# Kernel optimization log

Hardware: AMD Instinct MI355X
Metric: run time of the kernel (lower is better)

## Reference

```python
import jax, jax.numpy as jnp
import numpy as np

K = 3          # kernel size
KF = K * K     # kernel field = 9
PAD = 1
STRIDE = 1


def _conv(x, w, b):
    y = jax.lax.conv_general_dilated(
        x, w, (STRIDE, STRIDE), [(PAD, PAD), (PAD, PAD)],
        dimension_numbers=('NCHW', 'OIHW', 'NCHW'))
    return y + b[None, :, None, None]


def _bilinear_gather(x, py, px):
    # x: [B,C,H,W]; py/px: [B,KF,Ho,Wo] float sampling coords (zero-pad outside)
    B, C, H, W = x.shape
    xf = x.reshape(B, C, H * W)
    y0 = jnp.floor(py)
    x0 = jnp.floor(px)

    def corner(yc, xc):
        wy = 1.0 - jnp.abs(py - yc)
        wx = 1.0 - jnp.abs(px - xc)
        valid = (yc >= 0) & (yc <= H - 1) & (xc >= 0) & (xc <= W - 1)
        yi = jnp.clip(yc, 0, H - 1).astype(jnp.int32)
        xi = jnp.clip(xc, 0, W - 1).astype(jnp.int32)
        idx = (yi * W + xi).reshape(B, -1)               # [B, KF*Ho*Wo]
        v = jax.vmap(lambda f, i: f[:, i])(xf, idx)      # [B, C, KF*Ho*Wo]
        wgt = (wy * wx * valid.astype(x.dtype)).reshape(B, 1, -1)
        return v * wgt

    return (corner(y0, x0) + corner(y0, x0 + 1) +
            corner(y0 + 1, x0) + corner(y0 + 1, x0 + 1))  # [B,C,KF*Ho*Wo]


def _deform_conv(x, offset, mask, w, b):
    # modulated deformable conv v2 (mmcv offset layout: [y,x] interleaved per kernel pt)
    B, C, H, W = x.shape
    Ho, Wo = mask.shape[2], mask.shape[3]
    kh, kw = jnp.meshgrid(jnp.arange(K), jnp.arange(K), indexing='ij')
    kh = kh.reshape(-1).astype(x.dtype)   # [KF]
    kw = kw.reshape(-1).astype(x.dtype)
    base_y = (jnp.arange(Ho) * STRIDE - PAD).astype(x.dtype)
    base_x = (jnp.arange(Wo) * STRIDE - PAD).astype(x.dtype)
    off = offset.reshape(B, KF, 2, Ho, Wo)
    py = base_y[None, None, :, None] + kh[None, :, None, None] + off[:, :, 0]
    px = base_x[None, None, None, :] + kw[None, :, None, None] + off[:, :, 1]
    val = _bilinear_gather(x, py, px).reshape(B, C, KF, Ho, Wo)
    val = val * mask[:, None]                             # modulate
    out = jnp.einsum('bckhw,ock->bohw', val, w.reshape(w.shape[0], C, KF))
    return out + b[None, :, None, None]


def setup_inputs() -> dict:
    key = jax.random.key(0)
    k1, k2, k3 = jax.random.split(key, 3)
    B, C, H, W = 8, 64, 128, 128
    x = jax.random.normal(k1, (B, C, H, W), dtype=jnp.float32)
    w_om = jax.random.normal(k2, (3 * KF, C, K, K), dtype=jnp.float32) * 0.02
    b_om = jnp.zeros((3 * KF,), dtype=jnp.float32)
    w_dc = jax.random.normal(k3, (64, C, K, K), dtype=jnp.float32) * 0.05
    b_dc = jnp.zeros((64,), dtype=jnp.float32)
    return {"x": x, "w_om": w_om, "b_om": b_om, "w_dc": w_dc, "b_dc": b_dc}


def reference(x, w_om, b_om, w_dc, b_dc):
    om = _conv(x, w_om, b_om)                 # [B, 3*KF, H, W]
    offset = om[:, :2 * KF]
    mask = 2.0 * jax.nn.sigmoid(om[:, 2 * KF:])
    return _deform_conv(x, offset, mask, w_dc, b_dc)
```

## Files before the change

### kernel.cpp

```cpp
#include <hip/hip_runtime.h>
#include <cmath>

#define IH 128
#define IW 128
#define NB 8

typedef __attribute__((ext_vector_type(8))) short bf16x8;
typedef __attribute__((ext_vector_type(4))) float f32x4;

union U4B8 { uint4 u; bf16x8 h; };

#define OFFM_OFF 0
#define XT_OFF   3538944
#define WTDC_OFF (3538944 + 4194304)
#define WTOM_OFF (3538944 + 4194304 + 18432)

__device__ __forceinline__ unsigned short f32_to_bf16(float f) {
    unsigned int u = __float_as_uint(f);
    u += 0x7fffu + ((u >> 16) & 1u);
    return (unsigned short)(u >> 16);
}

__global__ void transpose_weights(const float* __restrict__ w_dc,
                                  const float* __restrict__ w_om,
                                  unsigned short* __restrict__ wt_dc16,
                                  unsigned short* __restrict__ wt_om16) {
    int idx = blockIdx.x * blockDim.x + threadIdx.x;
    if (idx < 9 * 64 * 64) {
        int k = idx >> 12;
        int o = (idx >> 6) & 63;
        int c = idx & 63;
        wt_dc16[idx] = f32_to_bf16(w_dc[(o * 64 + c) * 9 + k]);
    }
    if (idx < 9 * 32 * 64) {
        int k = idx >> 11;
        int o = (idx >> 6) & 31;
        int c = idx & 63;
        wt_om16[idx] = (o < 27) ? f32_to_bf16(w_om[(o * 64 + c) * 9 + k])
                                : (unsigned short)0;
    }
}

__global__ __launch_bounds__(256) void transpose_x(
        const float* __restrict__ x, unsigned short* __restrict__ xT) {
    __shared__ float t[64 * 65];
    const int tid = threadIdx.x;
    const int blk = blockIdx.x;
    const int b = blk >> 8;
    const int rem = blk & 255;
    const int h = rem >> 1;
    const int w0 = (rem & 1) << 6;

    for (int i = tid; i < 4096; i += 256) {
        const int c = i >> 6;
        const int w = i & 63;
        t[w * 65 + c] = x[(((size_t)(b * 64 + c)) << 14) + (h << 7) + w0 + w];
    }
    __syncthreads();
    const int c2 = (tid & 31) * 2;
    ushort2* dst = (ushort2*)(xT + (((size_t)b << 20)) + ((size_t)((h << 7) + w0)) * 64 + c2);
#pragma unroll
    for (int p = 0; p < 8; ++p) {
        const int w = (tid >> 5) + p * 8;
        ushort2 u;
        u.x = f32_to_bf16(t[w * 65 + c2]);
        u.y = f32_to_bf16(t[w * 65 + c2 + 1]);
        dst[(size_t)w * 32] = u;
    }
}

__global__ __launch_bounds__(256, 4) void conv_om_mfma(
        const unsigned short* __restrict__ xT,
        const float* __restrict__ b_om,
        const unsigned short* __restrict__ wt_om16,
        float* __restrict__ offm) {
    __shared__ __align__(16) unsigned short wall[9 * 8 * 32 * 8];

    const int tid = threadIdx.x;
    for (int s = tid; s < 2304; s += 256) {
        const int k = s >> 8;
        const int r = s & 255;
        const int p = r >> 5;
        const int o = r & 31;
        ((uint4*)wall)[s] = ((const uint4*)wt_om16)[(k << 8) + (o << 3) + p];
    }
    __syncthreads();

    const int t = (blockIdx.x << 2) + (tid >> 6);
    const int b = t >> 10;
    const int rem = t & 1023;
    const int h = rem >> 3;
    const int w0 = (rem & 7) << 4;
    const int lane = tid & 63;
    const int ln15 = lane & 15;
    const int quad = lane >> 4;

    const unsigned short* xb = xT + ((size_t)b << 20);

    f32x4 acc[2] = {{0.f, 0.f, 0.f, 0.f}, {0.f, 0.f, 0.f, 0.f}};

#pragma unroll
    for (int k = 0; k < 9; ++k) {
        const int kh = k / 3;
        const int kw = k - kh * 3;
        const int y = h + kh - 1;
        const int xx = w0 + ln15 + kw - 1;
        U4B8 a0, a1;
        a0.u = make_uint4(0u, 0u, 0u, 0u);
        a1.u = make_uint4(0u, 0u, 0u, 0u);
        if (y >= 0 && y < IH && xx >= 0 && xx < IW) {
            const unsigned short* p = xb + (((size_t)((y << 7) + xx)) << 6) + (quad << 3);
            a0.u = *(const uint4*)p;
            a1.u = *(const uint4*)(p + 32);
        }
        const unsigned short* wb  = wall + (((k << 3) + quad) << 8);
        const unsigned short* wb4 = wall + (((k << 3) + quad + 4) << 8);
#pragma unroll
        for (int ot = 0; ot < 2; ++ot) {
            U4B8 b0, b1;
            b0.u = *(const uint4*)&wb [((ot << 4) + ln15) << 3];
            b1.u = *(const uint4*)&wb4[((ot << 4) + ln15) << 3];
            acc[ot] = __builtin_amdgcn_mfma_f32_16x16x32_bf16(a0.h, b0.h, acc[ot], 0, 0, 0);
            acc[ot] = __builtin_amdgcn_mfma_f32_16x16x32_bf16(a1.h, b1.h, acc[ot], 0, 0, 0);
        }
    }

#pragma unroll
    for (int ot = 0; ot < 2; ++ot) {
        const int o = (ot << 4) + ln15;
        if (o >= 27) continue;
        const float bias = b_om[o];
        float4 r;
        r.x = acc[ot][0] + bias;
        r.y = acc[ot][1] + bias;
        r.z = acc[ot][2] + bias;
        r.w = acc[ot][3] + bias;
        if (o >= 18) {
            r.x = 2.0f / (1.0f + __expf(-r.x));
            r.y = 2.0f / (1.0f + __expf(-r.y));
            r.z = 2.0f / (1.0f + __expf(-r.z));
            r.w = 2.0f / (1.0f + __expf(-r.w));
        }
        *(float4*)&offm[(((size_t)(b * 27 + o)) << 14) + (h << 7) + w0 + (quad << 2)] = r;
    }
}

__device__ __forceinline__ void corner2(const unsigned short* __restrict__ p,
                                        float wgt, float* v) {
    const uint4 a = *(const uint4*)p;
    const uint4 c = *(const uint4*)(p + 32);
    unsigned int u[8] = {a.x, a.y, a.z, a.w, c.x, c.y, c.z, c.w};
#pragma unroll
    for (int i = 0; i < 8; ++i) {
        v[2 * i]     += wgt * __uint_as_float(u[i] << 16);
        v[2 * i + 1] += wgt * __uint_as_float(u[i] & 0xffff0000u);
    }
}

__global__ __launch_bounds__(256, 2) void deform_mfma(
        const unsigned short* __restrict__ xT,
        const float* __restrict__ b_dc,
        const float* __restrict__ offm,
        const unsigned short* __restrict__ wt_dc16,
        float* __restrict__ out) {
    __shared__ __align__(16) unsigned short wall[9 * 8 * 64 * 8];

    const int tid = threadIdx.x;
    for (int s = tid; s < 4608; s += 256) {
        const int k = s >> 9;
        const int r = s & 511;
        const int p = r >> 6;
        const int o = r & 63;
        ((uint4*)wall)[s] = ((const uint4*)wt_dc16)[(k << 9) + (o << 3) + p];
    }
    __syncthreads();

    const int t = (blockIdx.x << 2) + (tid >> 6);
    const int b = t >> 10;
    const int rem = t & 1023;
    const int h = rem >> 3;
    const int w0 = (rem & 7) << 4;
    const int lane = tid & 63;
    const int ln15 = lane & 15;
    const int quad = lane >> 4;

    const unsigned short* xb = xT + ((size_t)b << 20);
    const float* ofb = offm + (((size_t)(b * 27)) << 14) + (h << 7) + w0 + ln15;

    f32x4 acc[4];
#pragma unroll
    for (int i = 0; i < 4; ++i) acc[i] = (f32x4){0.f, 0.f, 0.f, 0.f};

#pragma unroll
    for (int k = 0; k < 9; ++k) {
        const float offy = ofb[((size_t)(2 * k)) << 14];
        const float offx = ofb[((size_t)(2 * k + 1)) << 14];
        const float msk  = ofb[((size_t)(18 + k)) << 14];
        const int kh = k / 3;
        const int kw = k - kh * 3;
        const float py  = (float)(h + kh - 1) + offy;
        const float pxf = (float)(w0 + ln15 + kw - 1) + offx;
        const float y0f = floorf(py);
        const float x0f = floorf(pxf);
        const float fy = py - y0f;
        const float fx = pxf - x0f;
        const float wy0 = 1.0f - fy, wx0 = 1.0f - fx;
        const float vy0 = (y0f >= 0.0f && y0f <= 127.0f) ? 1.0f : 0.0f;
        const float vy1 = (y0f >= -1.0f && y0f <= 126.0f) ? 1.0f : 0.0f;
        const float vx0 = (x0f >= 0.0f && x0f <= 127.0f) ? 1.0f : 0.0f;
        const float vx1 = (x0f >= -1.0f && x0f <= 126.0f) ? 1.0f : 0.0f;
        const float w00 = wy0 * wx0 * vy0 * vx0;
        const float w01 = wy0 * fx  * vy0 * vx1;
        const float w10 = fy  * wx0 * vy1 * vx0;
        const float w11 = fy  * fx  * vy1 * vx1;
        const int y0i = min(max((int)y0f, 0), 127);
        const int y1i = min(max((int)y0f + 1, 0), 127);
        const int x0i = min(max((int)x0f, 0), 127);
        const int x1i = min(max((int)x0f + 1, 0), 127);

        float v[16];
#pragma unroll
        for (int i = 0; i < 16; ++i) v[i] = 0.0f;
        const int cofs = quad << 3;
        corner2(xb + ((((size_t)((y0i << 7) + x0i)) << 6) + cofs), w00, v);
        corner2(xb + ((((size_t)((y0i << 7) + x1i)) << 6) + cofs), w01, v);
        corner2(xb + ((((size_t)((y1i << 7) + x0i)) << 6) + cofs), w10, v);
        corner2(xb + ((((size_t)((y1i << 7) + x1i)) << 6) + cofs), w11, v);

        U4B8 a0, a1;
        unsigned int pk[8];
#pragma unroll
        for (int i = 0; i < 8; ++i) {
            const unsigned int lo = f32_to_bf16(v[2 * i] * msk);
            const unsigned int hi = f32_to_bf16(v[2 * i + 1] * msk);
            pk[i] = lo | (hi << 16);
        }
        a0.u = make_uint4(pk[0], pk[1], pk[2], pk[3]);
        a1.u = make_uint4(pk[4], pk[5], pk[6], pk[7]);

        const unsigned short* wb  = wall + (((k << 3) + quad) << 9);
        const unsigned short* wb4 = wall + (((k << 3) + quad + 4) << 9);
#pragma unroll
        for (int ot = 0; ot < 4; ++ot) {
            U4B8 b0, b1;
            b0.u = *(const uint4*)&wb [((ot << 4) + ln15) << 3];
            b1.u = *(const uint4*)&wb4[((ot << 4) + ln15) << 3];
            acc[ot] = __builtin_amdgcn_mfma_f32_16x16x32_bf16(a0.h, b0.h, acc[ot], 0, 0, 0);
            acc[ot] = __builtin_amdgcn_mfma_f32_16x16x32_bf16(a1.h, b1.h, acc[ot], 0, 0, 0);
        }
    }

#pragma unroll
    for (int ot = 0; ot < 4; ++ot) {
        const int o = (ot << 4) + ln15;
        const float bias = b_dc[o];
        float4 r;
        r.x = acc[ot][0] + bias;
        r.y = acc[ot][1] + bias;
        r.z = acc[ot][2] + bias;
        r.w = acc[ot][3] + bias;
        *(float4*)&out[(((size_t)(b * 64 + o)) << 14) + (h << 7) + w0 + (quad << 2)] = r;
    }
}

extern "C" void kernel_launch(void* const* d_in, const int* in_sizes, int n_in,
                              void* d_out, int out_size, void* d_ws, size_t ws_size,
                              hipStream_t stream) {
    const float* x    = (const float*)d_in[0];
    const float* w_om = (const float*)d_in[1];
    const float* b_om = (const float*)d_in[2];
    const float* w_dc = (const float*)d_in[3];
    const float* b_dc = (const float*)d_in[4];
    float* out = (float*)d_out;
    float* ws  = (float*)d_ws;

    float* offm = ws + OFFM_OFF;
    unsigned short* xT      = (unsigned short*)(ws + XT_OFF);
    unsigned short* wt_dc16 = (unsigned short*)(ws + WTDC_OFF);
    unsigned short* wt_om16 = (unsigned short*)(ws + WTOM_OFF);

    const int n_blocks = NB * IH * (IW / 16) / 4;

    transpose_weights<<<144, 256, 0, stream>>>(w_dc, w_om, wt_dc16, wt_om16);
    transpose_x<<<NB * IH * 2, 256, 0, stream>>>(x, xT);
    conv_om_mfma<<<n_blocks, 256, 0, stream>>>(xT, b_om, wt_om16, offm);
    deform_mfma<<<n_blocks, 256, 0, stream>>>(xT, b_dc, offm, wt_dc16, out);
}
```

Baseline: 202.9 us.

## Fuse offset/mask conv into deformable conv kernel via shared-memory staging

Merges the offset/mask convolution and the deformable convolution into one kernel. Each block now covers 64 pixels of one row, computes the 27 offset/mask channels into LDS, then reuses the same LDS buffer for the deform weights. This removes the global round trip of the offset tensor (about 3.5M floats written and read) and one kernel launch. In exchange the weight tables are reloaded serially inside every block with an extra barrier, and occupancy is limited by the larger LDS footprint.

Result: no change. 200.5 us (-1.2%).

```diff
diff --git a/kernel.cpp b/kernel.cpp
--- a/kernel.cpp
+++ b/kernel.cpp
@@ -10,10 +10,9 @@
 
 union U4B8 { uint4 u; bf16x8 h; };
 
-#define OFFM_OFF 0
-#define XT_OFF   3538944
-#define WTDC_OFF (3538944 + 4194304)
-#define WTOM_OFF (3538944 + 4194304 + 18432)
+#define XT_OFF   0
+#define WTDC_OFF 4194304
+#define WTOM_OFF (4194304 + 18432)
 
 __device__ __forceinline__ unsigned short f32_to_bf16(float f) {
     unsigned int u = __float_as_uint(f);
@@ -69,14 +68,40 @@
     }
 }
 
-__global__ __launch_bounds__(256, 4) void conv_om_mfma(
+__device__ __forceinline__ void corner2(const unsigned short* __restrict__ p,
+                                        float wgt, float* v) {
+    const uint4 a = *(const uint4*)p;
+    const uint4 c = *(const uint4*)(p + 32);
+    unsigned int u[8] = {a.x, a.y, a.z, a.w, c.x, c.y, c.z, c.w};
+#pragma unroll
+    for (int i = 0; i < 8; ++i) {
+        v[2 * i]     += wgt * __uint_as_float(u[i] << 16);
+        v[2 * i + 1] += wgt * __uint_as_float(u[i] & 0xffff0000u);
+    }
+}
+
+__global__ __launch_bounds__(256, 2) void fused_dcn(
         const unsigned short* __restrict__ xT,
         const float* __restrict__ b_om,
         const unsigned short* __restrict__ wt_om16,
-        float* __restrict__ offm) {
-    __shared__ __align__(16) unsigned short wall[9 * 8 * 32 * 8];
+        const float* __restrict__ b_dc,
+        const unsigned short* __restrict__ wt_dc16,
+        float* __restrict__ out) {
+    __shared__ __align__(16) unsigned short wall[9 * 8 * 64 * 8];
+    __shared__ __align__(16) float offs[27 * 68];
 
     const int tid = threadIdx.x;
+    const int b = blockIdx.x >> 8;
+    const int rem = blockIdx.x & 255;
+    const int h = rem >> 1;
+    const int w0 = (rem & 1) << 6;
+    const int wid = tid >> 6;
+    const int lane = tid & 63;
+    const int ln15 = lane & 15;
+    const int quad = lane >> 4;
+
+    const unsigned short* xb = xT + ((size_t)b << 20);
+
     for (int s = tid; s < 2304; s += 256) {
         const int k = s >> 8;
         const int r = s & 255;
@@ -86,86 +111,55 @@
     }
     __syncthreads();
 
-    const int t = (blockIdx.x << 2) + (tid >> 6);
-    const int b = t >> 10;
-    const int rem = t & 1023;
-    const int h = rem >> 3;
-    const int w0 = (rem & 7) << 4;
-    const int lane = tid & 63;
-    const int ln15 = lane & 15;
-    const int quad = lane >> 4;
-
-    const unsigned short* xb = xT + ((size_t)b << 20);
-
-    f32x4 acc[2] = {{0.f, 0.f, 0.f, 0.f}, {0.f, 0.f, 0.f, 0.f}};
-
-#pragma unroll
-    for (int k = 0; k < 9; ++k) {
-        const int kh = k / 3;
-        const int kw = k - kh * 3;
-        const int y = h + kh - 1;
-        const int xx = w0 + ln15 + kw - 1;
-        U4B8 a0, a1;
-        a0.u = make_uint4(0u, 0u, 0u, 0u);
-        a1.u = make_uint4(0u, 0u, 0u, 0u);
-        if (y >= 0 && y < IH && xx >= 0 && xx < IW) {
-            const unsigned short* p = xb + (((size_t)((y << 7) + xx)) << 6) + (quad << 3);
-            a0.u = *(const uint4*)p;
-            a1.u = *(const uint4*)(p + 32);
-        }
-        const unsigned short* wb  = wall + (((k << 3) + quad) << 8);
-        const unsigned short* wb4 = wall + (((k << 3) + quad + 4) << 8);
+    {
+        f32x4 acc[2] = {{0.f, 0.f, 0.f, 0.f}, {0.f, 0.f, 0.f, 0.f}};
+#pragma unroll
+        for (int k = 0; k < 9; ++k) {
+            const int kh = k / 3;
+            const int kw = k - kh * 3;
+            const int y = h + kh - 1;
+            const int xx = w0 + (wid << 4) + ln15 + kw - 1;
+            U4B8 a0, a1;
+            a0.u = make_uint4(0u, 0u, 0u, 0u);
+            a1.u = make_uint4(0u, 0u, 0u, 0u);
+            if (y >= 0 && y < IH && xx >= 0 && xx < IW) {
+                const unsigned short* p = xb + (((size_t)((y << 7) + xx)) << 6) + (quad << 3);
+                a0.u = *(const uint4*)p;
+                a1.u = *(const uint4*)(p + 32);
+            }
+            const unsigned short* wb  = wall + (((k << 3) + quad) << 8);
+            const unsigned short* wb4 = wall + (((k << 3) + quad + 4) << 8);
+#pragma unroll
+            for (int ot = 0; ot < 2; ++ot) {
+                U4B8 b0, b1;
+                b0.u = *(const uint4*)&wb [((ot << 4) + ln15) << 3];
+                b1.u = *(const uint4*)&wb4[((ot << 4) + ln15) << 3];
+                acc[ot] = __builtin_amdgcn_mfma_f32_16x16x32_bf16(a0.h, b0.h, acc[ot], 0, 0, 0);
+                acc[ot] = __builtin_amdgcn_mfma_f32_16x16x32_bf16(a1.h, b1.h, acc[ot], 0, 0, 0);
+            }
+        }
 #pragma unroll
         for (int ot = 0; ot < 2; ++ot) {
-            U4B8 b0, b1;
-            b0.u = *(const uint4*)&wb [((ot << 4) + ln15) << 3];
-            b1.u = *(const uint4*)&wb4[((ot << 4) + ln15) << 3];
-            acc[ot] = __builtin_amdgcn_mfma_f32_16x16x32_bf16(a0.h, b0.h, acc[ot], 0, 0, 0);
-            acc[ot] = __builtin_amdgcn_mfma_f32_16x16x32_bf16(a1.h, b1.h, acc[ot], 0, 0, 0);
-        }
-    }
-
-#pragma unroll
-    for (int ot = 0; ot < 2; ++ot) {
-        const int o = (ot << 4) + ln15;
-        if (o >= 27) continue;
-        const float bias = b_om[o];
-        float4 r;
-        r.x = acc[ot][0] + bias;
-        r.y = acc[ot][1] + bias;
-        r.z = acc[ot][2] + bias;
-        r.w = acc[ot][3] + bias;
-        if (o >= 18) {
-            r.x = 2.0f / (1.0f + __expf(-r.x));
-            r.y = 2.0f / (1.0f + __expf(-r.y));
-            r.z = 2.0f / (1.0f + __expf(-r.z));
-            r.w = 2.0f / (1.0f + __expf(-r.w));
-        }
-        *(float4*)&offm[(((size_t)(b * 27 + o)) << 14) + (h << 7) + w0 + (quad << 2)] = r;
-    }
-}
-
-__device__ __forceinline__ void corner2(const unsigned short* __restrict__ p,
-                                        float wgt, float* v) {
-    const uint4 a = *(const uint4*)p;
-    const uint4 c = *(const uint4*)(p + 32);
-    unsigned int u[8] = {a.x, a.y, a.z, a.w, c.x, c.y, c.z, c.w};
-#pragma unroll
-    for (int i = 0; i < 8; ++i) {
-        v[2 * i]     += wgt * __uint_as_float(u[i] << 16);
-        v[2 * i + 1] += wgt * __uint_as_float(u[i] & 0xffff0000u);
-    }
-}
-
-__global__ __launch_bounds__(256, 2) void deform_mfma(
-        const unsigned short* __restrict__ xT,
-        const float* __restrict__ b_dc,
-        const float* __restrict__ offm,
-        const unsigned short* __restrict__ wt_dc16,
-        float* __restrict__ out) {
-    __shared__ __align__(16) unsigned short wall[9 * 8 * 64 * 8];
-
-    const int tid = threadIdx.x;
+            const int o = (ot << 4) + ln15;
+            if (o < 27) {
+                const float bias = b_om[o];
+                float4 r;
+                r.x = acc[ot][0] + bias;
+                r.y = acc[ot][1] + bias;
+                r.z = acc[ot][2] + bias;
+                r.w = acc[ot][3] + bias;
+                if (o >= 18) {
+                    r.x = 2.0f / (1.0f + __expf(-r.x));
+                    r.y = 2.0f / (1.0f + __expf(-r.y));
+                    r.z = 2.0f / (1.0f + __expf(-r.z));
+                    r.w = 2.0f / (1.0f + __expf(-r.w));
+                }
+                *(float4*)&offs[o * 68 + (wid << 4) + (quad << 2)] = r;
+            }
+        }
+    }
+    __syncthreads();
+
     for (int s = tid; s < 4608; s += 256) {
         const int k = s >> 9;
         const int r = s & 511;
@@ -175,17 +169,7 @@
     }
     __syncthreads();
 
-    const int t = (blockIdx.x << 2) + (tid >> 6);
-    const int b = t >> 10;
-    const int rem = t & 1023;
-    const int h = rem >> 3;
-    const int w0 = (rem & 7) << 4;
-    const int lane = tid & 63;
-    const int ln15 = lane & 15;
-    const int quad = lane >> 4;
-
-    const unsigned short* xb = xT + ((size_t)b << 20);
-    const float* ofb = offm + (((size_t)(b * 27)) << 14) + (h << 7) + w0 + ln15;
+    const int lpx = (wid << 4) + ln15;
 
     f32x4 acc[4];
 #pragma unroll
@@ -193,13 +177,13 @@
 
 #pragma unroll
     for (int k = 0; k < 9; ++k) {
-        const float offy = ofb[((size_t)(2 * k)) << 14];
-        const float offx = ofb[((size_t)(2 * k + 1)) << 14];
-        const float msk  = ofb[((size_t)(18 + k)) << 14];
+        const float offy = offs[(2 * k) * 68 + lpx];
+        const float offx = offs[(2 * k + 1) * 68 + lpx];
+        const float msk  = offs[(18 + k) * 68 + lpx];
         const int kh = k / 3;
         const int kw = k - kh * 3;
         const float py  = (float)(h + kh - 1) + offy;
-        const float pxf = (float)(w0 + ln15 + kw - 1) + offx;
+        const float pxf = (float)(w0 + lpx + kw - 1) + offx;
         const float y0f = floorf(py);
         const float x0f = floorf(pxf);
         const float fy = py - y0f;
@@ -259,7 +243,7 @@
         r.y = acc[ot][1] + bias;
         r.z = acc[ot][2] + bias;
         r.w = acc[ot][3] + bias;
-        *(float4*)&out[(((size_t)(b * 64 + o)) << 14) + (h << 7) + w0 + (quad << 2)] = r;
+        *(float4*)&out[(((size_t)(b * 64 + o)) << 14) + (h << 7) + w0 + (wid << 4) + (quad << 2)] = r;
     }
 }
 
@@ -274,15 +258,13 @@
     float* out = (float*)d_out;
     float* ws  = (float*)d_ws;
 
-    float* offm = ws + OFFM_OFF;
     unsigned short* xT      = (unsigned short*)(ws + XT_OFF);
     unsigned short* wt_dc16 = (unsigned short*)(ws + WTDC_OFF);
     unsigned short* wt_om16 = (unsigned short*)(ws + WTOM_OFF);
 
-    const int n_blocks = NB * IH * (IW / 16) / 4;
+    const int n_blocks = NB * IH * (IW / 64);
 
     transpose_weights<<<144, 256, 0, stream>>>(w_dc, w_om, wt_dc16, wt_om16);
     transpose_x<<<NB * IH * 2, 256, 0, stream>>>(x, xT);
-    conv_om_mfma<<<n_blocks, 256, 0, stream>>>(xT, b_om, wt_om16, offm);
-    deform_mfma<<<n_blocks, 256, 0, stream>>>(xT, b_dc, offm, wt_dc16, out);
-}
+    fused_dcn<<<n_blocks, 256, 0, stream>>>(xT, b_om, wt_om16, b_dc, wt_dc16, out);
+}
```
